# Performance work log

Hardware: AMD Instinct MI355X
Metric: run time of the kernel (lower is better)

The kernel has to match this reference:

```python
import jax, jax.numpy as jnp
import numpy as np

DIM = 1024
HEADS = 16
HEAD_DIM = DIM // HEADS
SCALE = HEAD_DIM ** -0.5


def setup_inputs() -> dict:
    key = jax.random.key(0)
    k1, k2, k3, k4 = jax.random.split(key, 4)
    x = jax.random.normal(k1, (2, 2048, DIM), dtype=jnp.float32)
    # nn.Linear(dim, 3*dim, bias=False): weight shape (3*dim, dim), y = x @ W.T
    w_qkv = jax.random.normal(k2, (3 * DIM, DIM), dtype=jnp.float32) * (DIM ** -0.5)
    w_proj = jax.random.normal(k3, (DIM, DIM), dtype=jnp.float32) * (DIM ** -0.5)
    head_w = jnp.ones((HEADS,), dtype=jnp.float32)
    return {"x": x, "w_qkv": w_qkv, "w_proj": w_proj, "head_w": head_w}


def reference(x, w_qkv, w_proj, head_w) -> jnp.ndarray:
    B, N, C = x.shape
    qkv = jnp.einsum("bnc,dc->bnd", x, w_qkv)  # [B,N,3C]
    qkv = qkv.reshape(B, N, 3, HEADS, HEAD_DIM).transpose(2, 0, 3, 1, 4)
    q, k, v = qkv[0], qkv[1], qkv[2]  # each [B,H,N,Dh]
    attn = jnp.einsum("bhqd,bhkd->bhqk", q, k) * SCALE  # [B,H,N,N]
    attn = jax.nn.softmax(attn, axis=-1)
    out = jnp.einsum("bhqk,bhkd->bhqd", attn, v)  # [B,H,N,Dh]
    hw = jax.nn.softmax(head_w)[None, :, None, None]
    out = out * hw
    out = out.transpose(0, 2, 1, 3).reshape(B, N, C)
    return jnp.einsum("bnc,dc->bnd", out, w_proj)
```

## Files before the change

kernel.cpp:

```cpp
#include <hip/hip_runtime.h>

typedef _Float16 half_t;
typedef _Float16 half8 __attribute__((ext_vector_type(8)));
typedef _Float16 half4_t __attribute__((ext_vector_type(4)));
typedef float floatx4 __attribute__((ext_vector_type(4)));
typedef float floatx16 __attribute__((ext_vector_type(16)));

#define B_SZ 2
#define SEQ 2048
#define DIM_ 1024
#define NH 16
#define DH 64
#define ROWS (B_SZ * SEQ)

__device__ __forceinline__ void gl2lds16(const void* g, void* l) {
  __builtin_amdgcn_global_load_lds((const __attribute__((address_space(1))) unsigned int*)g,
                                   (__attribute__((address_space(3))) unsigned int*)l, 16, 0, 0);
}

__global__ __launch_bounds__(256) void convert_all(const float4* __restrict__ x,
                                                   const float4* __restrict__ wq,
                                                   const float4* __restrict__ wp,
                                                   half4_t* __restrict__ dst,
                                                   int nx, int nq, int np) {
  int i = blockIdx.x * blockDim.x + threadIdx.x;
  float4 v;
  if (i < nx) v = x[i];
  else if (i < nx + nq) v = wq[i - nx];
  else if (i < nx + nq + np) v = wp[i - nx - nq];
  else return;
  half4_t h;
  h.x = (half_t)v.x; h.y = (half_t)v.y; h.z = (half_t)v.z; h.w = (half_t)v.w;
  dst[i] = h;
}

template <int MODE, int BN>
__global__ __launch_bounds__(256) void gemm32(const half_t* __restrict__ A,
                                              const half_t* __restrict__ Bt,
                                              half_t* __restrict__ q16,
                                              half_t* __restrict__ k16,
                                              half_t* __restrict__ vT16,
                                              float* __restrict__ outp) {
  constexpr int K = 1024;
  constexpr int NT = BN / 64;
  __shared__ __align__(16) half_t a_lds[128 * 64];
  __shared__ __align__(16) half_t b_lds[BN * 64];
  const int t = threadIdx.x;
  const int wave = t >> 6, lane = t & 63;
  const int l31 = lane & 31, hw = lane >> 5;
  const int wm = wave >> 1, wn = wave & 1;
  const int row0 = blockIdx.y * 128, col0 = blockIdx.x * BN;

  floatx16 acc[2][NT];
#pragma unroll
  for (int i = 0; i < 2; ++i)
#pragma unroll
    for (int j = 0; j < NT; ++j)
#pragma unroll
      for (int r = 0; r < 16; ++r) acc[i][j][r] = 0.f;

  for (int k0 = 0; k0 < K; k0 += 64) {
#pragma unroll
    for (int hi = 0; hi < 4; ++hi) {
      int s = t + hi * 256;
      int row = s >> 3, c = s & 7;
      int sc = c ^ (row & 7);
      gl2lds16(A + (size_t)(row0 + row) * K + (k0 + sc * 8), a_lds + (wave * 64 + hi * 256) * 8);
    }
#pragma unroll
    for (int hi = 0; hi < BN / 32; ++hi) {
      int s = t + hi * 256;
      int row = s >> 3, c = s & 7;
      int sc = c ^ (row & 7);
      gl2lds16(Bt + (size_t)(col0 + row) * K + (k0 + sc * 8), b_lds + (wave * 64 + hi * 256) * 8);
    }
    __syncthreads();
    half8 af[2][4], bf[NT][4];
#pragma unroll
    for (int mt = 0; mt < 2; ++mt) {
      int row = wm * 64 + mt * 32 + l31;
#pragma unroll
      for (int kf = 0; kf < 4; ++kf)
        af[mt][kf] = *(const half8*)(a_lds + row * 64 + ((kf * 2 + hw) ^ (row & 7)) * 8);
    }
#pragma unroll
    for (int nt = 0; nt < NT; ++nt) {
      int row = wn * (BN / 2) + nt * 32 + l31;
#pragma unroll
      for (int kf = 0; kf < 4; ++kf)
        bf[nt][kf] = *(const half8*)(b_lds + row * 64 + ((kf * 2 + hw) ^ (row & 7)) * 8);
    }
#pragma unroll
    for (int kf = 0; kf < 4; ++kf)
#pragma unroll
      for (int mt = 0; mt < 2; ++mt)
#pragma unroll
        for (int nt = 0; nt < NT; ++nt)
          acc[mt][nt] =
              __builtin_amdgcn_mfma_f32_32x32x16_f16(af[mt][kf], bf[nt][kf], acc[mt][nt], 0, 0, 0);
    __syncthreads();
  }

  if (MODE == 0) {
    const int which = col0 >> 10;
#pragma unroll
    for (int mt = 0; mt < 2; ++mt)
#pragma unroll
      for (int nt = 0; nt < NT; ++nt) {
        int growb = row0 + wm * 64 + mt * 32;
        int gcol = col0 + wn * (BN / 2) + nt * 32 + l31;
        int hc = gcol & 1023, h = hc >> 6, d = hc & 63;
        if (which == 2) {
#pragma unroll
          for (int rq = 0; rq < 4; ++rq) {
            int grow = growb + 8 * rq + 4 * hw;
            int b = grow >> 11, n0 = grow & 2047;
            int bh = b * NH + h;
            half4_t h4;
            h4.x = (half_t)acc[mt][nt][rq * 4 + 0];
            h4.y = (half_t)acc[mt][nt][rq * 4 + 1];
            h4.z = (half_t)acc[mt][nt][rq * 4 + 2];
            h4.w = (half_t)acc[mt][nt][rq * 4 + 3];
            *(half4_t*)(vT16 + ((size_t)bh * DH + d) * SEQ + n0) = h4;
          }
        } else {
#pragma unroll
          for (int r = 0; r < 16; ++r) {
            int grow = growb + (r & 3) + 8 * (r >> 2) + 4 * hw;
            int b = grow >> 11, n = grow & 2047;
            int bh = b * NH + h;
            float v = acc[mt][nt][r];
            if (which == 0)
              q16[((size_t)bh * SEQ + n) * DH + d] = (half_t)(v * 0.125f);
            else
              k16[((size_t)bh * SEQ + n) * DH + d] = (half_t)v;
          }
        }
      }
  } else {
#pragma unroll
    for (int mt = 0; mt < 2; ++mt)
#pragma unroll
      for (int nt = 0; nt < NT; ++nt) {
        int growb = row0 + wm * 64 + mt * 32;
        int gcol = col0 + wn * (BN / 2) + nt * 32 + l31;
#pragma unroll
        for (int r = 0; r < 16; ++r) {
          int grow = growb + (r & 3) + 8 * (r >> 2) + 4 * hw;
          outp[(size_t)grow * DIM_ + gcol] = acc[mt][nt][r];
        }
      }
  }
}

__global__ __launch_bounds__(256) void attn_p1(const half_t* __restrict__ q16,
                                               const half_t* __restrict__ k16,
                                               const half_t* __restrict__ vT16,
                                               half_t* __restrict__ opart,
                                               float* __restrict__ psums) {
  __shared__ __align__(16) half_t k_lds[2][64 * 64];
  __shared__ __align__(16) half_t v_lds[2][64 * 64];

  const int t = threadIdx.x;
  const int wave = t >> 6, lane = t & 63;
  const int l15 = lane & 15, quad = lane >> 4;
  const int blk = blockIdx.x;
  const int js = blk & 1, qt = (blk >> 1) & 15, bh = blk >> 5;
  const half_t* qp = q16 + (size_t)bh * SEQ * DH;
  const half_t* kp = k16 + (size_t)bh * SEQ * DH;
  const half_t* vp = vT16 + (size_t)bh * DH * SEQ;
  const int q0w = qt * 128 + wave * 32;
  const int jbase = js * 1024;

  const int s0 = t, s1 = t + 256;
  const int r0_ = s0 >> 3, c0_ = (s0 & 7) ^ (r0_ & 7);
  const int r1_ = s1 >> 3, c1_ = (s1 & 7) ^ (r1_ & 7);

  half8 qf[2][2];
#pragma unroll
  for (int mi = 0; mi < 2; ++mi)
#pragma unroll
    for (int kf = 0; kf < 2; ++kf)
      qf[mi][kf] = *(const half8*)(qp + (size_t)(q0w + mi * 16 + l15) * DH + kf * 32 + quad * 8);

  const floatx4 z4 = {0.f, 0.f, 0.f, 0.f};
  floatx4 o[2][4];
  float psum[2] = {0.f, 0.f};
#pragma unroll
  for (int mi = 0; mi < 2; ++mi)
#pragma unroll
    for (int i = 0; i < 4; ++i) o[mi][i] = z4;

  gl2lds16(kp + (size_t)(jbase + r0_) * DH + c0_ * 8, &k_lds[0][(wave * 64) * 8]);
  gl2lds16(vp + (size_t)r0_ * SEQ + jbase + c0_ * 8, &v_lds[0][(wave * 64) * 8]);
  gl2lds16(kp + (size_t)(jbase + r1_) * DH + c1_ * 8, &k_lds[0][(wave * 64 + 256) * 8]);
  gl2lds16(vp + (size_t)r1_ * SEQ + jbase + c1_ * 8, &v_lds[0][(wave * 64 + 256) * 8]);

  int cur = 0;
  for (int jt = 0; jt < 16; ++jt) {
    __syncthreads();

    if (jt + 1 < 16) {
      const int j0 = jbase + (jt + 1) * 64, nb = cur ^ 1;
      gl2lds16(kp + (size_t)(j0 + r0_) * DH + c0_ * 8, &k_lds[nb][(wave * 64) * 8]);
      gl2lds16(vp + (size_t)r0_ * SEQ + j0 + c0_ * 8, &v_lds[nb][(wave * 64) * 8]);
      gl2lds16(kp + (size_t)(j0 + r1_) * DH + c1_ * 8, &k_lds[nb][(wave * 64 + 256) * 8]);
      gl2lds16(vp + (size_t)r1_ * SEQ + j0 + c1_ * 8, &v_lds[nb][(wave * 64 + 256) * 8]);
    }

    const half_t* kl = k_lds[cur];
    const half_t* vl = v_lds[cur];

    floatx4 st[2][4];
#pragma unroll
    for (int mi = 0; mi < 2; ++mi)
#pragma unroll
      for (int nt = 0; nt < 4; ++nt) st[mi][nt] = z4;
#pragma unroll
    for (int kf = 0; kf < 2; ++kf)
#pragma unroll
      for (int nt = 0; nt < 4; ++nt) {
        int row = nt * 16 + l15;
        half8 kb = *(const half8*)(kl + row * 64 + (((kf << 2) | quad) ^ (row & 7)) * 8);
        st[0][nt] = __builtin_amdgcn_mfma_f32_16x16x32_f16(kb, qf[0][kf], st[0][nt], 0, 0, 0);
        st[1][nt] = __builtin_amdgcn_mfma_f32_16x16x32_f16(kb, qf[1][kf], st[1][nt], 0, 0, 0);
      }

    half4_t pf[2][4];
#pragma unroll
    for (int mi = 0; mi < 2; ++mi)
#pragma unroll
      for (int nt = 0; nt < 4; ++nt) {
        float p0 = __expf(st[mi][nt][0]);
        float p1 = __expf(st[mi][nt][1]);
        float p2 = __expf(st[mi][nt][2]);
        float p3 = __expf(st[mi][nt][3]);
        psum[mi] += (p0 + p1) + (p2 + p3);
        half4_t pk;
        pk.x = (half_t)p0; pk.y = (half_t)p1; pk.z = (half_t)p2; pk.w = (half_t)p3;
        pf[mi][nt] = pk;
      }

#pragma unroll
    for (int jt2 = 0; jt2 < 4; ++jt2)
#pragma unroll
      for (int dt = 0; dt < 4; ++dt) {
        int row = dt * 16 + l15;
        int ch = (jt2 * 2 + (quad >> 1)) ^ (l15 & 7);
        half4_t vb = *(const half4_t*)(vl + row * 64 + ch * 8 + (quad & 1) * 4);
        o[0][dt] = __builtin_amdgcn_mfma_f32_16x16x16f16(pf[0][jt2], vb, o[0][dt], 0, 0, 0);
        o[1][dt] = __builtin_amdgcn_mfma_f32_16x16x16f16(pf[1][jt2], vb, o[1][dt], 0, 0, 0);
      }
    cur ^= 1;
  }

#pragma unroll
  for (int mi = 0; mi < 2; ++mi) {
    psum[mi] += __shfl_xor(psum[mi], 16, 64);
    psum[mi] += __shfl_xor(psum[mi], 32, 64);
  }
  if (quad == 0) {
#pragma unroll
    for (int mi = 0; mi < 2; ++mi)
      psums[((size_t)(js * 32 + bh)) * SEQ + q0w + mi * 16 + l15] = psum[mi];
  }

#pragma unroll
  for (int mi = 0; mi < 2; ++mi)
#pragma unroll
    for (int r = 0; r < 4; ++r) {
      int n = q0w + mi * 16 + quad * 4 + r;
      size_t base = ((size_t)(js * 32 + bh) * SEQ + n) * DH;
#pragma unroll
      for (int dt = 0; dt < 4; ++dt)
        opart[base + dt * 16 + l15] = (half_t)o[mi][dt][r];
    }
}

__global__ __launch_bounds__(256) void combine(const half_t* __restrict__ opart,
                                               const float* __restrict__ psums,
                                               const float* __restrict__ head_w,
                                               half_t* __restrict__ attn16) {
  int idx = blockIdx.x * blockDim.x + threadIdx.x;
  int d4 = idx & 15, n = (idx >> 4) & 2047, bh = idx >> 15;
  int h = bh & 15, b = bh >> 4;
  const size_t jstr = (size_t)32 * SEQ * DH;
  size_t off = ((size_t)bh * SEQ + n) * DH + d4 * 4;
  half4_t o0 = *(const half4_t*)(opart + off);
  half4_t o1 = *(const half4_t*)(opart + jstr + off);
  float ps = psums[(size_t)bh * SEQ + n] + psums[(size_t)32 * SEQ + (size_t)bh * SEQ + n];

  float mw = head_w[0];
#pragma unroll
  for (int i = 1; i < NH; ++i) mw = fmaxf(mw, head_w[i]);
  float sw = 0.f;
#pragma unroll
  for (int i = 0; i < NH; ++i) sw += __expf(head_w[i] - mw);
  float hwv = __expf(head_w[h] - mw) / sw;

  float scl = hwv / ps;
  half4_t r;
  r.x = (half_t)(((float)o0.x + (float)o1.x) * scl);
  r.y = (half_t)(((float)o0.y + (float)o1.y) * scl);
  r.z = (half_t)(((float)o0.z + (float)o1.z) * scl);
  r.w = (half_t)(((float)o0.w + (float)o1.w) * scl);
  *(half4_t*)(attn16 + ((size_t)(b * SEQ + n)) * DIM_ + h * DH + d4 * 4) = r;
}

extern "C" void kernel_launch(void* const* d_in, const int* in_sizes, int n_in,
                              void* d_out, int out_size, void* d_ws, size_t ws_size,
                              hipStream_t stream) {
  const float* x = (const float*)d_in[0];
  const float* w_qkv = (const float*)d_in[1];
  const float* w_proj = (const float*)d_in[2];
  const float* head_w = (const float*)d_in[3];
  float* out = (float*)d_out;

  half_t* x16 = (half_t*)d_ws;
  half_t* wq16 = x16 + (size_t)ROWS * DIM_;
  half_t* wp16 = wq16 + (size_t)3 * DIM_ * DIM_;
  half_t* q16 = wp16 + (size_t)DIM_ * DIM_;
  half_t* k16 = q16 + (size_t)ROWS * DIM_;
  half_t* vT16 = k16 + (size_t)ROWS * DIM_;
  half_t* attn16 = vT16 + (size_t)ROWS * DIM_;
  half_t* opart = attn16 + (size_t)ROWS * DIM_;
  float* psums = (float*)(opart + (size_t)2 * 32 * SEQ * DH);

  const int nx = ROWS * DIM_ / 4, nq = 3 * DIM_ * DIM_ / 4, np = DIM_ * DIM_ / 4;
  convert_all<<<(nx + nq + np) / 256, 256, 0, stream>>>((const float4*)x, (const float4*)w_qkv,
                                                        (const float4*)w_proj, (half4_t*)x16,
                                                        nx, nq, np);

  gemm32<0, 128><<<dim3(24, 32), 256, 0, stream>>>(x16, wq16, q16, k16, vT16, nullptr);
  attn_p1<<<32 * 16 * 2, 256, 0, stream>>>(q16, k16, vT16, opart, psums);
  combine<<<(32 * SEQ * DH / 4) / 256, 256, 0, stream>>>(opart, psums, head_w, attn16);
  gemm32<1, 64><<<dim3(16, 32), 256, 0, stream>>>(attn16, wp16, nullptr, nullptr, nullptr, out);
}
```

Measured before the change: 199.7 us.

## Double per-wave query tile in attention and compute row sums via MFMA

Each wave in the attention kernel now handles 64 queries instead of 32, so every K/V tile loaded into LDS is reused across twice as many query rows, and the grid is halved. The softmax row sum is now computed by an extra MFMA against a ones vector instead of scalar adds plus shuffles. Exp becomes exp2, with log2(e) folded into the Q scale. Conversion uses packed cvt_pkrtz, and s_setprio is placed around the MFMA blocks. Register pressure rises sharply (o[4][4], pf[4][4], qf[4][2]) and there are fewer blocks (512), which may reduce occupancy and latency hiding.

Result: faster. 195.4 us (-2.1%).

```diff
diff --git a/kernel.cpp b/kernel.cpp
--- a/kernel.cpp
+++ b/kernel.cpp
@@ -3,6 +3,7 @@
 typedef _Float16 half_t;
 typedef _Float16 half8 __attribute__((ext_vector_type(8)));
 typedef _Float16 half4_t __attribute__((ext_vector_type(4)));
+typedef _Float16 half2_t __attribute__((ext_vector_type(2)));
 typedef float floatx4 __attribute__((ext_vector_type(4)));
 typedef float floatx16 __attribute__((ext_vector_type(16)));
 
@@ -16,6 +17,28 @@
 __device__ __forceinline__ void gl2lds16(const void* g, void* l) {
   __builtin_amdgcn_global_load_lds((const __attribute__((address_space(1))) unsigned int*)g,
                                    (__attribute__((address_space(3))) unsigned int*)l, 16, 0, 0);
+}
+
+__device__ __forceinline__ float fexp2(float x) {
+#if __has_builtin(__builtin_amdgcn_exp2f)
+  return __builtin_amdgcn_exp2f(x);
+#else
+  return __expf(x * 0.6931471805599453f);
+#endif
+}
+
+__device__ __forceinline__ half4_t pack4(float p0, float p1, float p2, float p3) {
+#if __has_builtin(__builtin_amdgcn_cvt_pkrtz)
+  half2_t lo = __builtin_bit_cast(half2_t, __builtin_amdgcn_cvt_pkrtz(p0, p1));
+  half2_t hi = __builtin_bit_cast(half2_t, __builtin_amdgcn_cvt_pkrtz(p2, p3));
+  half4_t r;
+  r.x = lo.x; r.y = lo.y; r.z = hi.x; r.w = hi.y;
+  return r;
+#else
+  half4_t r;
+  r.x = (half_t)p0; r.y = (half_t)p1; r.z = (half_t)p2; r.w = (half_t)p3;
+  return r;
+#endif
 }
 
 __global__ __launch_bounds__(256) void convert_all(const float4* __restrict__ x,
@@ -131,7 +154,8 @@
             int bh = b * NH + h;
             float v = acc[mt][nt][r];
             if (which == 0)
-              q16[((size_t)bh * SEQ + n) * DH + d] = (half_t)(v * 0.125f);
+              q16[((size_t)bh * SEQ + n) * DH + d] =
+                  (half_t)(v * 0.1803368801111204f);
             else
               k16[((size_t)bh * SEQ + n) * DH + d] = (half_t)v;
           }
@@ -165,31 +189,35 @@
   const int wave = t >> 6, lane = t & 63;
   const int l15 = lane & 15, quad = lane >> 4;
   const int blk = blockIdx.x;
-  const int js = blk & 1, qt = (blk >> 1) & 15, bh = blk >> 5;
+  const int js = blk & 1, qt = (blk >> 1) & 7, bh = blk >> 4;
   const half_t* qp = q16 + (size_t)bh * SEQ * DH;
   const half_t* kp = k16 + (size_t)bh * SEQ * DH;
   const half_t* vp = vT16 + (size_t)bh * DH * SEQ;
-  const int q0w = qt * 128 + wave * 32;
+  const int q0w = qt * 256 + wave * 64;
   const int jbase = js * 1024;
 
   const int s0 = t, s1 = t + 256;
   const int r0_ = s0 >> 3, c0_ = (s0 & 7) ^ (r0_ & 7);
   const int r1_ = s1 >> 3, c1_ = (s1 & 7) ^ (r1_ & 7);
 
-  half8 qf[2][2];
-#pragma unroll
-  for (int mi = 0; mi < 2; ++mi)
+  half8 qf[4][2];
+#pragma unroll
+  for (int mi = 0; mi < 4; ++mi)
 #pragma unroll
     for (int kf = 0; kf < 2; ++kf)
       qf[mi][kf] = *(const half8*)(qp + (size_t)(q0w + mi * 16 + l15) * DH + kf * 32 + quad * 8);
 
   const floatx4 z4 = {0.f, 0.f, 0.f, 0.f};
-  floatx4 o[2][4];
-  float psum[2] = {0.f, 0.f};
-#pragma unroll
-  for (int mi = 0; mi < 2; ++mi)
+  floatx4 o[4][4];
+  floatx4 oex[4];
+#pragma unroll
+  for (int mi = 0; mi < 4; ++mi) {
+    oex[mi] = z4;
 #pragma unroll
     for (int i = 0; i < 4; ++i) o[mi][i] = z4;
+  }
+  half4_t vones;
+  vones.x = (half_t)1.f; vones.y = (half_t)1.f; vones.z = (half_t)1.f; vones.w = (half_t)1.f;
 
   gl2lds16(kp + (size_t)(jbase + r0_) * DH + c0_ * 8, &k_lds[0][(wave * 64) * 8]);
   gl2lds16(vp + (size_t)r0_ * SEQ + jbase + c0_ * 8, &v_lds[0][(wave * 64) * 8]);
@@ -211,62 +239,61 @@
     const half_t* kl = k_lds[cur];
     const half_t* vl = v_lds[cur];
 
-    floatx4 st[2][4];
-#pragma unroll
-    for (int mi = 0; mi < 2; ++mi)
-#pragma unroll
-      for (int nt = 0; nt < 4; ++nt) st[mi][nt] = z4;
-#pragma unroll
-    for (int kf = 0; kf < 2; ++kf)
-#pragma unroll
-      for (int nt = 0; nt < 4; ++nt) {
-        int row = nt * 16 + l15;
-        half8 kb = *(const half8*)(kl + row * 64 + (((kf << 2) | quad) ^ (row & 7)) * 8);
-        st[0][nt] = __builtin_amdgcn_mfma_f32_16x16x32_f16(kb, qf[0][kf], st[0][nt], 0, 0, 0);
-        st[1][nt] = __builtin_amdgcn_mfma_f32_16x16x32_f16(kb, qf[1][kf], st[1][nt], 0, 0, 0);
+    half4_t pf[4][4];
+#pragma unroll
+    for (int nt = 0; nt < 4; ++nt) {
+      const int row = nt * 16 + l15;
+      half8 kb0 = *(const half8*)(kl + row * 64 + ((0 | quad) ^ (row & 7)) * 8);
+      half8 kb1 = *(const half8*)(kl + row * 64 + ((4 | quad) ^ (row & 7)) * 8);
+      floatx4 st[4];
+      __builtin_amdgcn_s_setprio(1);
+#pragma unroll
+      for (int mi = 0; mi < 4; ++mi)
+        st[mi] = __builtin_amdgcn_mfma_f32_16x16x32_f16(kb0, qf[mi][0], z4, 0, 0, 0);
+#pragma unroll
+      for (int mi = 0; mi < 4; ++mi)
+        st[mi] = __builtin_amdgcn_mfma_f32_16x16x32_f16(kb1, qf[mi][1], st[mi], 0, 0, 0);
+      __builtin_amdgcn_s_setprio(0);
+#pragma unroll
+      for (int mi = 0; mi < 4; ++mi) {
+        float p0 = fexp2(st[mi][0]);
+        float p1 = fexp2(st[mi][1]);
+        float p2 = fexp2(st[mi][2]);
+        float p3 = fexp2(st[mi][3]);
+        pf[mi][nt] = pack4(p0, p1, p2, p3);
       }
-
-    half4_t pf[2][4];
-#pragma unroll
-    for (int mi = 0; mi < 2; ++mi)
-#pragma unroll
-      for (int nt = 0; nt < 4; ++nt) {
-        float p0 = __expf(st[mi][nt][0]);
-        float p1 = __expf(st[mi][nt][1]);
-        float p2 = __expf(st[mi][nt][2]);
-        float p3 = __expf(st[mi][nt][3]);
-        psum[mi] += (p0 + p1) + (p2 + p3);
-        half4_t pk;
-        pk.x = (half_t)p0; pk.y = (half_t)p1; pk.z = (half_t)p2; pk.w = (half_t)p3;
-        pf[mi][nt] = pk;
-      }
-
-#pragma unroll
-    for (int jt2 = 0; jt2 < 4; ++jt2)
+    }
+
+    __builtin_amdgcn_s_setprio(1);
+#pragma unroll
+    for (int jt2 = 0; jt2 < 4; ++jt2) {
 #pragma unroll
       for (int dt = 0; dt < 4; ++dt) {
         int row = dt * 16 + l15;
         int ch = (jt2 * 2 + (quad >> 1)) ^ (l15 & 7);
         half4_t vb = *(const half4_t*)(vl + row * 64 + ch * 8 + (quad & 1) * 4);
-        o[0][dt] = __builtin_amdgcn_mfma_f32_16x16x16f16(pf[0][jt2], vb, o[0][dt], 0, 0, 0);
-        o[1][dt] = __builtin_amdgcn_mfma_f32_16x16x16f16(pf[1][jt2], vb, o[1][dt], 0, 0, 0);
+#pragma unroll
+        for (int mi = 0; mi < 4; ++mi)
+          o[mi][dt] = __builtin_amdgcn_mfma_f32_16x16x16f16(pf[mi][jt2], vb, o[mi][dt], 0, 0, 0);
       }
+#pragma unroll
+      for (int mi = 0; mi < 4; ++mi)
+        oex[mi] = __builtin_amdgcn_mfma_f32_16x16x16f16(pf[mi][jt2], vones, oex[mi], 0, 0, 0);
+    }
+    __builtin_amdgcn_s_setprio(0);
     cur ^= 1;
   }
 
-#pragma unroll
-  for (int mi = 0; mi < 2; ++mi) {
-    psum[mi] += __shfl_xor(psum[mi], 16, 64);
-    psum[mi] += __shfl_xor(psum[mi], 32, 64);
-  }
-  if (quad == 0) {
-#pragma unroll
-    for (int mi = 0; mi < 2; ++mi)
-      psums[((size_t)(js * 32 + bh)) * SEQ + q0w + mi * 16 + l15] = psum[mi];
-  }
-
-#pragma unroll
-  for (int mi = 0; mi < 2; ++mi)
+  if (l15 == 0) {
+#pragma unroll
+    for (int mi = 0; mi < 4; ++mi)
+#pragma unroll
+      for (int r = 0; r < 4; ++r)
+        psums[((size_t)(js * 32 + bh)) * SEQ + q0w + mi * 16 + quad * 4 + r] = oex[mi][r];
+  }
+
+#pragma unroll
+  for (int mi = 0; mi < 4; ++mi)
 #pragma unroll
     for (int r = 0; r < 4; ++r) {
       int n = q0w + mi * 16 + quad * 4 + r;
@@ -332,7 +359,7 @@
                                                         nx, nq, np);
 
   gemm32<0, 128><<<dim3(24, 32), 256, 0, stream>>>(x16, wq16, q16, k16, vT16, nullptr);
-  attn_p1<<<32 * 16 * 2, 256, 0, stream>>>(q16, k16, vT16, opart, psums);
+  attn_p1<<<32 * 8 * 2, 256, 0, stream>>>(q16, k16, vT16, opart, psums);
   combine<<<(32 * SEQ * DH / 4) / 256, 256, 0, stream>>>(opart, psums, head_w, attn16);
   gemm32<1, 64><<<dim3(16, 32), 256, 0, stream>>>(attn16, wp16, nullptr, nullptr, nullptr, out);
 }
```
